# Optimization experiments

Measured on AMD Instinct MI355X. Metric: run time of the kernel, lower is better.

## Reference

```python
import jax, jax.numpy as jnp
import numpy as np

NUM_HEADS = 8
LN_EPS = 1e-5


def _layernorm(x, g, b):
    m = jnp.mean(x, axis=-1, keepdims=True)
    v = jnp.mean(jnp.square(x - m), axis=-1, keepdims=True)
    return (x - m) * jax.lax.rsqrt(v + LN_EPS) * g + b


def setup_inputs() -> dict:
    key = jax.random.key(0)
    ks = jax.random.split(key, 10)
    D, C, Cin = 2, 256, 64  # depth, embed dim, input channels
    w = lambda k, shape: jax.random.normal(k, shape, jnp.float32) * 0.02
    return {
        "x": jax.random.normal(ks[0], (4, Cin, 12, 12, 12), jnp.float32),
        "W_pe": w(ks[1], (Cin, C)),
        "b_pe": jnp.zeros((C,), jnp.float32),
        "cls_token": w(ks[2], (1, 1, C)),
        "ln1_g": jnp.ones((D, C), jnp.float32),
        "ln1_b": jnp.zeros((D, C), jnp.float32),
        "Wqkv": w(ks[3], (D, C, 3 * C)),
        "Wproj": w(ks[4], (D, C, C)),
        "bproj": jnp.zeros((D, C), jnp.float32),
        "ln2_g": jnp.ones((D, C), jnp.float32),
        "ln2_b": jnp.zeros((D, C), jnp.float32),
        "W1": w(ks[5], (D, C, C)),
        "b1": jnp.zeros((D, C), jnp.float32),
        "W2": w(ks[6], (D, C, C)),
        "b2": jnp.zeros((D, C), jnp.float32),
        "normf_g": jnp.ones((C,), jnp.float32),
        "normf_b": jnp.zeros((C,), jnp.float32),
    }


def reference(x, W_pe, b_pe, cls_token, ln1_g, ln1_b, Wqkv, Wproj, bproj,
              ln2_g, ln2_b, W1, b1, W2, b2, normf_g, normf_b):
    B, Cin, H, W, L = x.shape
    C = W_pe.shape[1]
    hd = C // NUM_HEADS
    scale = hd ** (-0.5)

    # PatchEmbed: 1x1x1 Conv3d == per-voxel linear projection, then flatten to tokens
    tok = jnp.einsum('bchwl,cd->bhwld', x, W_pe).reshape(B, H * W * L, C) + b_pe
    cls = jnp.broadcast_to(cls_token, (B, 1, C))
    t = jnp.concatenate([cls, tok], axis=1)  # [B, N, C], N = H*W*L + 1
    N = t.shape[1]

    depth = Wqkv.shape[0]
    for i in range(depth):
        # --- self-attention ---
        y = _layernorm(t, ln1_g[i], ln1_b[i])
        qkv = (y @ Wqkv[i]).reshape(B, N, 3, NUM_HEADS, hd)
        qkv = jnp.transpose(qkv, (2, 0, 3, 1, 4))  # [3, B, H, N, hd]
        q, k, v = qkv[0], qkv[1], qkv[2]
        attn = jnp.einsum('bhnd,bhmd->bhnm', q, k) * scale
        attn = jax.nn.softmax(attn, axis=-1)
        o = jnp.einsum('bhnm,bhmd->bhnd', attn, v)
        o = jnp.transpose(o, (0, 2, 1, 3)).reshape(B, N, C)
        t = t + (o @ Wproj[i] + bproj[i])
        # --- MLP (mlp_ratio=1.0, exact GELU) ---
        y = _layernorm(t, ln2_g[i], ln2_b[i])
        h = jax.nn.gelu(y @ W1[i] + b1[i], approximate=False)
        t = t + (h @ W2[i] + b2[i])

    t = _layernorm(t, normf_g, normf_b)
    x_cls = t[:, 0]                                   # [B, C]
    feat = t[:, 1:]                                   # [B, H*W*L, C]
    feat = jnp.transpose(feat, (0, 2, 1)).reshape(B, C, H, W, L)  # downsample = Identity for dim=256
    return x_cls, feat
```

## Files before the change

kernel.cpp:

```cpp
#include <hip/hip_runtime.h>
#include <hip/hip_bf16.h>
#include <math.h>

#define B_   4
#define CIN  64
#define P_   1728
#define N_   1729
#define C_   256
#define NH_  8
#define HD_  32
#define M_   (B_*N_)
#define NPAD 1792

typedef __bf16 bf16x8 __attribute__((ext_vector_type(8)));
typedef __bf16 bf16x4 __attribute__((ext_vector_type(4)));
typedef float  f32x4  __attribute__((ext_vector_type(4)));

__global__ __launch_bounds__(256) void embed2(
    const float* __restrict__ x, const float* __restrict__ Wpe,
    const float* __restrict__ bpe, const float* __restrict__ cls,
    float* __restrict__ t)
{
    int idx = blockIdx.x*256 + threadIdx.x;
    int c   = idx & 255;
    int n   = (idx >> 8) % N_;
    int b   = idx / (N_*256);
    if (n == 0) { t[idx] = cls[c]; return; }
    int p = n - 1;
    float acc = bpe[c];
    for (int ci = 0; ci < CIN; ++ci)
        acc += x[(size_t)(b*CIN + ci)*P_ + p] * Wpe[ci*C_ + c];
    t[idx] = acc;
}

__global__ __launch_bounds__(256) void ln4(
    const float* __restrict__ in, __bf16* __restrict__ out,
    const float* __restrict__ g, const float* __restrict__ bb)
{
    int wv = threadIdx.x >> 6, lane = threadIdx.x & 63;
    size_t row = (size_t)blockIdx.x*4 + wv;
    float4 v = *(const float4*)&in[row*C_ + lane*4];
    float s1 = (v.x+v.y)+(v.z+v.w);
    float s2 = (v.x*v.x+v.y*v.y)+(v.z*v.z+v.w*v.w);
    #pragma unroll
    for (int off = 32; off >= 1; off >>= 1) {
        s1 += __shfl_xor(s1, off);
        s2 += __shfl_xor(s2, off);
    }
    float mean = s1*(1.0f/C_);
    float var  = fmaxf(s2*(1.0f/C_) - mean*mean, 0.0f);
    float rstd = rsqrtf(var + 1e-5f);
    float4 gg = *(const float4*)&g[lane*4];
    float4 bv = *(const float4*)&bb[lane*4];
    bf16x4 r;
    r[0] = (__bf16)((v.x-mean)*rstd*gg.x + bv.x);
    r[1] = (__bf16)((v.y-mean)*rstd*gg.y + bv.y);
    r[2] = (__bf16)((v.z-mean)*rstd*gg.z + bv.z);
    r[3] = (__bf16)((v.w-mean)*rstd*gg.w + bv.w);
    *(bf16x4*)&out[row*C_ + lane*4] = r;
}

__global__ __launch_bounds__(256) void ln4f(
    const float* __restrict__ in, float* __restrict__ out,
    const float* __restrict__ g, const float* __restrict__ bb,
    float* __restrict__ cls_out)
{
    int wv = threadIdx.x >> 6, lane = threadIdx.x & 63;
    size_t row = (size_t)blockIdx.x*4 + wv;
    float4 v = *(const float4*)&in[row*C_ + lane*4];
    float s1 = (v.x+v.y)+(v.z+v.w);
    float s2 = (v.x*v.x+v.y*v.y)+(v.z*v.z+v.w*v.w);
    #pragma unroll
    for (int off = 32; off >= 1; off >>= 1) {
        s1 += __shfl_xor(s1, off);
        s2 += __shfl_xor(s2, off);
    }
    float mean = s1*(1.0f/C_);
    float var  = fmaxf(s2*(1.0f/C_) - mean*mean, 0.0f);
    float rstd = rsqrtf(var + 1e-5f);
    float4 gg = *(const float4*)&g[lane*4];
    float4 bv = *(const float4*)&bb[lane*4];
    float4 r;
    r.x = (v.x-mean)*rstd*gg.x + bv.x;
    r.y = (v.y-mean)*rstd*gg.y + bv.y;
    r.z = (v.z-mean)*rstd*gg.z + bv.z;
    r.w = (v.w-mean)*rstd*gg.w + bv.w;
    *(float4*)&out[row*C_ + lane*4] = r;
    if ((row % N_) == 0)
        *(float4*)&cls_out[(row / N_)*C_ + lane*4] = r;
}

__global__ __launch_bounds__(256) void wprep2(
    const float* __restrict__ Wqkv, const float* __restrict__ Wproj,
    const float* __restrict__ W1,   const float* __restrict__ W2,
    __bf16* __restrict__ wT)
{
    int z = blockIdx.z, which = z >> 1, layer = z & 1;
    const float* src; __bf16* dst; int NC;
    if (which == 0) {
        src = Wqkv + (size_t)layer*C_*768;
        dst = wT   + (size_t)layer*768*256;
        NC  = 768;
    } else {
        NC = 256;
        const float* b3 = (which == 1) ? Wproj : (which == 2) ? W1 : W2;
        src = b3 + (size_t)layer*65536;
        dst = wT + 2*768*256 + (size_t)((which-1)*2 + layer)*65536;
    }
    int n0 = blockIdx.x*32; if (n0 >= NC) return;
    int k0 = blockIdx.y*32;
    __shared__ float tile[32][33];
    int c = threadIdx.x & 31, r = threadIdx.x >> 5;
    for (int rr = r; rr < 32; rr += 8)
        tile[rr][c] = src[(size_t)(k0+rr)*NC + n0 + c];
    __syncthreads();
    for (int rr = r; rr < 32; rr += 8)
        dst[(size_t)(n0+rr)*256 + k0 + c] = (__bf16)tile[c][rr];
}

template<int NC, bool ADD, bool GELU, bool BIAS, bool OUTBF>
__global__ __launch_bounds__(256) void gemm3(
    const __bf16* __restrict__ A, const __bf16* __restrict__ Wt,
    const float* __restrict__ bias, float* __restrict__ outF,
    __bf16* __restrict__ outB)
{
    __shared__ __align__(16) __bf16 As[64*32];
    __shared__ __align__(16) __bf16 Bs[64*32];
    int r0 = blockIdx.x*64, c0 = blockIdx.y*64;
    int tid = threadIdx.x;
    int wv = tid >> 6, lane = tid & 63, quad = lane >> 4, mn = lane & 15;
    int sr = tid >> 2, sc = tid & 3;
    int ga = r0 + sr; if (ga >= M_) ga = M_ - 1;

    f32x4 acc[4];
    #pragma unroll
    for (int ct = 0; ct < 4; ++ct)
        #pragma unroll
        for (int rr = 0; rr < 4; ++rr) acc[ct][rr] = 0.f;

    for (int kc = 0; kc < 8; ++kc) {
        __syncthreads();
        *(bf16x8*)&As[sr*32 + ((sc ^ (sr & 3))*8)] =
            *(const bf16x8*)&A[(size_t)ga*256 + kc*32 + sc*8];
        *(bf16x8*)&Bs[sr*32 + ((sc ^ (sr & 3))*8)] =
            *(const bf16x8*)&Wt[(size_t)(c0+sr)*256 + kc*32 + sc*8];
        __syncthreads();

        bf16x8 a = *(const bf16x8*)&As[(wv*16 + mn)*32 + ((quad ^ (mn & 3))*8)];
        #pragma unroll
        for (int ct = 0; ct < 4; ++ct) {
            bf16x8 b = *(const bf16x8*)&Bs[(ct*16 + mn)*32 + ((quad ^ (mn & 3))*8)];
            acc[ct] = __builtin_amdgcn_mfma_f32_16x16x32_bf16(a, b, acc[ct], 0, 0, 0);
        }
    }

    #pragma unroll
    for (int ct = 0; ct < 4; ++ct) {
        int col = c0 + ct*16 + mn;
        #pragma unroll
        for (int rr = 0; rr < 4; ++rr) {
            int row = r0 + wv*16 + quad*4 + rr;
            if (row >= M_) continue;
            float val = acc[ct][rr];
            if (BIAS) val += bias[col];
            if (GELU) val = 0.5f*val*(1.f + erff(val*0.70710678118654752f));
            size_t oi = (size_t)row*NC + col;
            if (OUTBF) outB[oi] = (__bf16)val;
            else if (ADD) outF[oi] += val;
            else outF[oi] = val;
        }
    }
}

__global__ __launch_bounds__(256) void gemm_qkv3(
    const __bf16* __restrict__ A, const __bf16* __restrict__ Wt,
    __bf16* __restrict__ qB, __bf16* __restrict__ kB, __bf16* __restrict__ vB)
{
    __shared__ __align__(16) __bf16 As[64*32];
    __shared__ __align__(16) __bf16 Bs[64*32];
    int r0 = blockIdx.x*64, c0 = blockIdx.y*64;
    int tid = threadIdx.x;
    int wv = tid >> 6, lane = tid & 63, quad = lane >> 4, mn = lane & 15;
    int sr = tid >> 2, sc = tid & 3;
    int ga = r0 + sr; if (ga >= M_) ga = M_ - 1;

    f32x4 acc[4];
    #pragma unroll
    for (int ct = 0; ct < 4; ++ct)
        #pragma unroll
        for (int rr = 0; rr < 4; ++rr) acc[ct][rr] = 0.f;

    for (int kc = 0; kc < 8; ++kc) {
        __syncthreads();
        *(bf16x8*)&As[sr*32 + ((sc ^ (sr & 3))*8)] =
            *(const bf16x8*)&A[(size_t)ga*256 + kc*32 + sc*8];
        *(bf16x8*)&Bs[sr*32 + ((sc ^ (sr & 3))*8)] =
            *(const bf16x8*)&Wt[(size_t)(c0+sr)*256 + kc*32 + sc*8];
        __syncthreads();

        bf16x8 a = *(const bf16x8*)&As[(wv*16 + mn)*32 + ((quad ^ (mn & 3))*8)];
        #pragma unroll
        for (int ct = 0; ct < 4; ++ct) {
            bf16x8 b = *(const bf16x8*)&Bs[(ct*16 + mn)*32 + ((quad ^ (mn & 3))*8)];
            acc[ct] = __builtin_amdgcn_mfma_f32_16x16x32_bf16(a, b, acc[ct], 0, 0, 0);
        }
    }

    const float scale = 0.17677669529663687f;
    #pragma unroll
    for (int ct = 0; ct < 4; ++ct) {
        int col = c0 + ct*16 + mn;
        #pragma unroll
        for (int rr = 0; rr < 4; ++rr) {
            int row = r0 + wv*16 + quad*4 + rr;
            if (row >= M_) continue;
            int b = row / N_, n = row - b*N_;
            float val = acc[ct][rr];
            if (col < 256) {
                int h = col >> 5, dd = col & 31;
                qB[((size_t)(b*NH_+h)*NPAD + n)*32 + dd] = (__bf16)(val*scale);
            } else if (col < 512) {
                int h = (col-256) >> 5, dd = col & 31;
                kB[((size_t)(b*NH_+h)*NPAD + n)*32 + dd] = (__bf16)val;
            } else {
                int h = (col-512) >> 5, dd = col & 31;
                vB[((size_t)(b*NH_+h)*32 + dd)*NPAD + n] = (__bf16)val;
            }
        }
    }
}

__global__ __launch_bounds__(256) void attn8(
    const __bf16* __restrict__ qB, const __bf16* __restrict__ kB,
    const __bf16* __restrict__ vB, __bf16* __restrict__ o)
{
    int bh = blockIdx.x, b = bh >> 3, h = bh & 7;
    int q0 = blockIdx.y * 64;
    int tid = threadIdx.x;
    int wv = tid >> 6, lane = tid & 63, quad = lane >> 4, mn = lane & 15;

    __shared__ __align__(16) __bf16 lk[64*32];
    __shared__ __align__(16) __bf16 lvt[32*64];
    __shared__ __align__(16) __bf16 lp[4][16*72];

    bf16x8 qfrag = *(const bf16x8*)(
        qB + ((size_t)bh*NPAD + q0 + wv*16 + mn)*32 + quad*8);

    bf16x8 vones;
    #pragma unroll
    for (int j = 0; j < 8; ++j) vones[j] = (mn == 0) ? (__bf16)1.0f : (__bf16)0.0f;

    f32x4 oacc0, oacc1, oacc2;
    #pragma unroll
    for (int rr = 0; rr < 4; ++rr) { oacc0[rr]=0.f; oacc1[rr]=0.f; oacc2[rr]=0.f; }

    const __bf16* kbase = kB + (size_t)bh*NPAD*32;
    const __bf16* vbase = vB + (size_t)bh*32*NPAD;
    int sr = tid >> 2, sc = tid & 3;
    int vr = tid >> 3, vc = tid & 7;

    for (int t = 0; t < 28; ++t) {
        int k0 = t*64;
        __syncthreads();
        *(bf16x8*)&lk[sr*32 + ((sc ^ (sr & 3))*8)] =
            *(const bf16x8*)(kbase + (size_t)(k0 + sr)*32 + sc*8);
        *(bf16x8*)&lvt[vr*64 + ((vc ^ (vr & 7))*8)] =
            *(const bf16x8*)(vbase + (size_t)vr*NPAD + k0 + vc*8);
        __syncthreads();

        f32x4 s[4];
        #pragma unroll
        for (int ct = 0; ct < 4; ++ct) {
            bf16x8 kf = *(const bf16x8*)&lk[(ct*16 + mn)*32 + ((quad ^ (mn & 3))*8)];
            f32x4 z;
            #pragma unroll
            for (int rr = 0; rr < 4; ++rr) z[rr] = 0.f;
            s[ct] = __builtin_amdgcn_mfma_f32_16x16x32_bf16(qfrag, kf, z, 0, 0, 0);
        }

        #pragma unroll
        for (int ct = 0; ct < 4; ++ct) {
            bool valid = (k0 + ct*16 + mn) < N_;
            #pragma unroll
            for (int rr = 0; rr < 4; ++rr) {
                float p = valid ? __expf(s[ct][rr]) : 0.f;
                lp[wv][(quad*4+rr)*72 + ct*16 + mn] = (__bf16)p;
            }
        }

        #pragma unroll
        for (int kh = 0; kh < 2; ++kh) {
            bf16x8 pf = *(const bf16x8*)&lp[wv][mn*72 + kh*32 + quad*8];
            int vsw = ((kh*4 + quad) ^ (mn & 7)) * 8;
            bf16x8 v0 = *(const bf16x8*)&lvt[ mn      *64 + vsw];
            bf16x8 v1 = *(const bf16x8*)&lvt[(mn+16)*64 + vsw];
            oacc0 = __builtin_amdgcn_mfma_f32_16x16x32_bf16(pf, v0, oacc0, 0, 0, 0);
            oacc1 = __builtin_amdgcn_mfma_f32_16x16x32_bf16(pf, v1, oacc1, 0, 0, 0);
            oacc2 = __builtin_amdgcn_mfma_f32_16x16x32_bf16(pf, vones, oacc2, 0, 0, 0);
        }
    }

    #pragma unroll
    for (int rr = 0; rr < 4; ++rr) {
        float l = __shfl(oacc2[rr], lane & 48);
        int q = q0 + wv*16 + quad*4 + rr;
        if (q >= N_) continue;
        float inv = 1.0f / l;
        size_t base = ((size_t)(b*N_ + q))*C_ + h*HD_;
        o[base + mn]      = (__bf16)(oacc0[rr]*inv);
        o[base + 16 + mn] = (__bf16)(oacc1[rr]*inv);
    }
}

__global__ __launch_bounds__(256) void feat3(
    const float* __restrict__ y, float* __restrict__ outf)
{
    __shared__ float tl[32][33];
    int p0 = blockIdx.x*32, c0 = blockIdx.y*32, b = blockIdx.z;
    int cc = threadIdx.x & 31, rr = threadIdx.x >> 5;
    for (int i = rr; i < 32; i += 8)
        tl[i][cc] = y[((size_t)(b*N_) + 1 + p0 + i)*C_ + c0 + cc];
    __syncthreads();
    for (int i = rr; i < 32; i += 8)
        outf[((size_t)(b*C_) + c0 + i)*P_ + p0 + cc] = tl[cc][i];
}

extern "C" void kernel_launch(void* const* d_in, const int* in_sizes, int n_in,
                              void* d_out, int out_size, void* d_ws, size_t ws_size,
                              hipStream_t stream)
{
    const float* x        = (const float*)d_in[0];
    const float* W_pe     = (const float*)d_in[1];
    const float* b_pe     = (const float*)d_in[2];
    const float* cls_tok  = (const float*)d_in[3];
    const float* ln1_g    = (const float*)d_in[4];
    const float* ln1_b    = (const float*)d_in[5];
    const float* Wqkv     = (const float*)d_in[6];
    const float* Wproj    = (const float*)d_in[7];
    const float* bproj    = (const float*)d_in[8];
    const float* ln2_g    = (const float*)d_in[9];
    const float* ln2_b    = (const float*)d_in[10];
    const float* W1       = (const float*)d_in[11];
    const float* b1       = (const float*)d_in[12];
    const float* W2       = (const float*)d_in[13];
    const float* b2       = (const float*)d_in[14];
    const float* normf_g  = (const float*)d_in[15];
    const float* normf_b  = (const float*)d_in[16];

    const size_t MC = (size_t)M_*C_;
    float*  ws  = (float*)d_ws;
    float*  t   = ws;
    float*  yf  = ws + MC;
    __bf16* ybf = (__bf16*)(ws + 2*MC);
    __bf16* hbf = (__bf16*)(ws + 2*MC + MC/2);
    __bf16* obf = (__bf16*)(ws + 2*MC + MC);
    __bf16* wT  = (__bf16*)(ws + 2*MC + 3*(MC/2));
    __bf16* qB  = wT + 2*768*256 + 6*256*256;
    __bf16* kB  = qB + (size_t)B_*NH_*NPAD*32;
    __bf16* vB  = kB + (size_t)B_*NH_*NPAD*32;

    __bf16* projT = wT + 2*768*256;
    __bf16* w1T   = projT + 2*256*256;
    __bf16* w2T   = w1T   + 2*256*256;

    float* out_cls  = (float*)d_out;
    float* out_feat = out_cls + B_*C_;

    wprep2<<<dim3(24, 8, 8), 256, 0, stream>>>(Wqkv, Wproj, W1, W2, wT);
    embed2<<<(B_*N_*C_)/256, 256, 0, stream>>>(x, W_pe, b_pe, cls_tok, t);

    const int GRID_M = (M_ + 63) / 64;
    for (int i = 0; i < 2; ++i) {
        ln4<<<M_/4, 256, 0, stream>>>(t, ybf, ln1_g + i*C_, ln1_b + i*C_);
        gemm_qkv3<<<dim3(GRID_M, 12), 256, 0, stream>>>(
            ybf, wT + (size_t)i*768*256, qB, kB, vB);
        attn8<<<dim3(32, 28), 256, 0, stream>>>(qB, kB, vB, obf);
        gemm3<256,true,false,true,false><<<dim3(GRID_M, 4), 256, 0, stream>>>(
            obf, projT + (size_t)i*65536, bproj + i*C_, t, nullptr);
        ln4<<<M_/4, 256, 0, stream>>>(t, ybf, ln2_g + i*C_, ln2_b + i*C_);
        gemm3<256,false,true,true,true><<<dim3(GRID_M, 4), 256, 0, stream>>>(
            ybf, w1T + (size_t)i*65536, b1 + i*C_, nullptr, hbf);
        gemm3<256,true,false,true,false><<<dim3(GRID_M, 4), 256, 0, stream>>>(
            hbf, w2T + (size_t)i*65536, b2 + i*C_, t, nullptr);
    }

    ln4f<<<M_/4, 256, 0, stream>>>(t, yf, normf_g, normf_b, out_cls);
    feat3<<<dim3(54, 8, 4), 256, 0, stream>>>(yf, out_feat);
}
```

Before: 318.6 us.

## Keep attention probabilities in registers via transposed S and 16x16x16 MFMA for PV

The attention kernel now computes S transposed (K as the A operand), so each lane's output is directly usable as a bf16x4 B-operand for a 16x16x16 MFMA against V. This removes the shared-memory staging of P and its extra reads. The row sum moves from an extra MFMA against a ones vector to a per-lane running sum reduced with shuffles. The output is transposed through LDS so it can be written with 16-byte vector stores. The trade-off is twice as many smaller MFMAs for the PV product and extra syncthreads in the epilogue.

```diff
diff --git a/kernel.cpp b/kernel.cpp
--- a/kernel.cpp
+++ b/kernel.cpp
@@ -15,6 +15,14 @@
 typedef __bf16 bf16x8 __attribute__((ext_vector_type(8)));
 typedef __bf16 bf16x4 __attribute__((ext_vector_type(4)));
 typedef float  f32x4  __attribute__((ext_vector_type(4)));
+
+#if __has_builtin(__builtin_amdgcn_mfma_f32_16x16x16_bf16)
+#define MFMA16(A,B,C) __builtin_amdgcn_mfma_f32_16x16x16_bf16(A,B,C,0,0,0)
+#else
+typedef short s16x4 __attribute__((ext_vector_type(4)));
+#define MFMA16(A,B,C) __builtin_amdgcn_mfma_f32_16x16x16bf16_1k( \
+    __builtin_bit_cast(s16x4,(A)), __builtin_bit_cast(s16x4,(B)), (C), 0,0,0)
+#endif
 
 __global__ __launch_bounds__(256) void embed2(
     const float* __restrict__ x, const float* __restrict__ Wpe,
@@ -230,7 +238,7 @@
     }
 }
 
-__global__ __launch_bounds__(256) void attn8(
+__global__ __launch_bounds__(256) void attn9(
     const __bf16* __restrict__ qB, const __bf16* __restrict__ kB,
     const __bf16* __restrict__ vB, __bf16* __restrict__ o)
 {
@@ -241,18 +249,14 @@
 
     __shared__ __align__(16) __bf16 lk[64*32];
     __shared__ __align__(16) __bf16 lvt[32*64];
-    __shared__ __align__(16) __bf16 lp[4][16*72];
 
     bf16x8 qfrag = *(const bf16x8*)(
         qB + ((size_t)bh*NPAD + q0 + wv*16 + mn)*32 + quad*8);
 
-    bf16x8 vones;
-    #pragma unroll
-    for (int j = 0; j < 8; ++j) vones[j] = (mn == 0) ? (__bf16)1.0f : (__bf16)0.0f;
-
-    f32x4 oacc0, oacc1, oacc2;
-    #pragma unroll
-    for (int rr = 0; rr < 4; ++rr) { oacc0[rr]=0.f; oacc1[rr]=0.f; oacc2[rr]=0.f; }
+    f32x4 oaccA, oaccB;
+    #pragma unroll
+    for (int rr = 0; rr < 4; ++rr) { oaccA[rr]=0.f; oaccB[rr]=0.f; }
+    float lsum = 0.f;
 
     const __bf16* kbase = kB + (size_t)bh*NPAD*32;
     const __bf16* vbase = vB + (size_t)bh*32*NPAD;
@@ -268,47 +272,52 @@
             *(const bf16x8*)(vbase + (size_t)vr*NPAD + k0 + vc*8);
         __syncthreads();
 
-        f32x4 s[4];
         #pragma unroll
         for (int ct = 0; ct < 4; ++ct) {
             bf16x8 kf = *(const bf16x8*)&lk[(ct*16 + mn)*32 + ((quad ^ (mn & 3))*8)];
             f32x4 z;
             #pragma unroll
             for (int rr = 0; rr < 4; ++rr) z[rr] = 0.f;
-            s[ct] = __builtin_amdgcn_mfma_f32_16x16x32_bf16(qfrag, kf, z, 0, 0, 0);
-        }
-
-        #pragma unroll
-        for (int ct = 0; ct < 4; ++ct) {
-            bool valid = (k0 + ct*16 + mn) < N_;
+            f32x4 st = __builtin_amdgcn_mfma_f32_16x16x32_bf16(kf, qfrag, z, 0, 0, 0);
+
+            bf16x4 pf;
             #pragma unroll
             for (int rr = 0; rr < 4; ++rr) {
-                float p = valid ? __expf(s[ct][rr]) : 0.f;
-                lp[wv][(quad*4+rr)*72 + ct*16 + mn] = (__bf16)p;
+                bool valid = (k0 + ct*16 + quad*4 + rr) < N_;
+                float p = valid ? __expf(st[rr]) : 0.f;
+                pf[rr] = (__bf16)p;
+                lsum += p;
             }
-        }
-
-        #pragma unroll
-        for (int kh = 0; kh < 2; ++kh) {
-            bf16x8 pf = *(const bf16x8*)&lp[wv][mn*72 + kh*32 + quad*8];
-            int vsw = ((kh*4 + quad) ^ (mn & 7)) * 8;
-            bf16x8 v0 = *(const bf16x8*)&lvt[ mn      *64 + vsw];
-            bf16x8 v1 = *(const bf16x8*)&lvt[(mn+16)*64 + vsw];
-            oacc0 = __builtin_amdgcn_mfma_f32_16x16x32_bf16(pf, v0, oacc0, 0, 0, 0);
-            oacc1 = __builtin_amdgcn_mfma_f32_16x16x32_bf16(pf, v1, oacc1, 0, 0, 0);
-            oacc2 = __builtin_amdgcn_mfma_f32_16x16x32_bf16(pf, vones, oacc2, 0, 0, 0);
-        }
-    }
-
-    #pragma unroll
-    for (int rr = 0; rr < 4; ++rr) {
-        float l = __shfl(oacc2[rr], lane & 48);
-        int q = q0 + wv*16 + quad*4 + rr;
-        if (q >= N_) continue;
-        float inv = 1.0f / l;
-        size_t base = ((size_t)(b*N_ + q))*C_ + h*HD_;
-        o[base + mn]      = (__bf16)(oacc0[rr]*inv);
-        o[base + 16 + mn] = (__bf16)(oacc1[rr]*inv);
+
+            int chunk = ct*2 + (quad >> 1);
+            int sub   = (quad & 1) * 4;
+            bf16x4 vloA = *(const bf16x4*)&lvt[ mn      *64 + ((chunk ^ (mn & 7))*8) + sub];
+            bf16x4 vloB = *(const bf16x4*)&lvt[(mn+16)*64 + ((chunk ^ (mn & 7))*8) + sub];
+            oaccA = MFMA16(vloA, pf, oaccA);
+            oaccB = MFMA16(vloB, pf, oaccB);
+        }
+    }
+
+    lsum += __shfl_xor(lsum, 16);
+    lsum += __shfl_xor(lsum, 32);
+    float inv = 1.0f / lsum;
+
+    __syncthreads();
+    {
+        int qrel = wv*16 + mn;
+        #pragma unroll
+        for (int rr = 0; rr < 4; ++rr) {
+            lk[qrel*32 + quad*4 + rr]      = (__bf16)(oaccA[rr]*inv);
+            lk[qrel*32 + 16 + quad*4 + rr] = (__bf16)(oaccB[rr]*inv);
+        }
+    }
+    __syncthreads();
+    {
+        int r = tid >> 2, ch = tid & 3;
+        int q = q0 + r;
+        if (q < N_)
+            *(bf16x8*)&o[((size_t)(b*N_ + q))*C_ + h*HD_ + ch*8] =
+                *(const bf16x8*)&lk[r*32 + ch*8];
     }
 }
 
@@ -374,7 +383,7 @@
         ln4<<<M_/4, 256, 0, stream>>>(t, ybf, ln1_g + i*C_, ln1_b + i*C_);
         gemm_qkv3<<<dim3(GRID_M, 12), 256, 0, stream>>>(
             ybf, wT + (size_t)i*768*256, qB, kB, vB);
-        attn8<<<dim3(32, 28), 256, 0, stream>>>(qB, kB, vB, obf);
+        attn9<<<dim3(32, 28), 256, 0, stream>>>(qB, kB, vB, obf);
         gemm3<256,true,false,true,false><<<dim3(GRID_M, 4), 256, 0, stream>>>(
             obf, projT + (size_t)i*65536, bproj + i*C_, t, nullptr);
         ln4<<<M_/4, 256, 0, stream>>>(t, ybf, ln2_g + i*C_, ln2_b + i*C_);
```

After: 330.4 us. +3.7%, slower.
